# Kernel optimization log

Measured on AMD Instinct MI355X. Metric: run time of the kernel, lower is better.

## Reference

```python
import jax, jax.numpy as jnp
import numpy as np

MODEL_DIM = 2048
Q_HEADS = 32
KV_HEADS = 8
HEAD_DIM = MODEL_DIM // Q_HEADS  # 64
ROPE_BASE = 10000.0


def apply_rope(x, pos):
    # x: [B, S, H, D], interleaved-pair RoPE (torchtune-style)
    half = x.shape[-1] // 2
    inv_freq = 1.0 / (ROPE_BASE ** (jnp.arange(half, dtype=jnp.float32) * 2.0 / x.shape[-1]))
    ang = pos.astype(jnp.float32)[:, None] * inv_freq[None, :]        # [S, half]
    cos = jnp.cos(ang)[None, :, None, :]                              # [1,S,1,half]
    sin = jnp.sin(ang)[None, :, None, :]
    x1 = x[..., 0::2]
    x2 = x[..., 1::2]
    o1 = x1 * cos - x2 * sin
    o2 = x2 * cos + x1 * sin
    return jnp.stack([o1, o2], axis=-1).reshape(x.shape)


def setup_inputs() -> dict:
    key = jax.random.key(0)
    ks = jax.random.split(key, 5)
    B, S, D = 2, 2048, MODEL_DIM
    sd = 1.0 / np.sqrt(D)
    x = jax.random.normal(ks[0], (B, S, D), dtype=jnp.float32)
    wq = jax.random.normal(ks[1], (Q_HEADS * HEAD_DIM, D), dtype=jnp.float32) * sd
    wk = jax.random.normal(ks[2], (KV_HEADS * HEAD_DIM, D), dtype=jnp.float32) * sd
    wv = jax.random.normal(ks[3], (KV_HEADS * HEAD_DIM, D), dtype=jnp.float32) * sd
    wo = jax.random.normal(ks[4], (D, D), dtype=jnp.float32) * sd
    attention_mask = jnp.ones((B, S), dtype=bool)
    return {"x": x, "attention_mask": attention_mask, "wq": wq, "wk": wk, "wv": wv, "wo": wo}


def reference(x, attention_mask, wq, wk, wv, wo):
    B, S, D = x.shape
    rep = Q_HEADS // KV_HEADS
    q = (x @ wq.T).reshape(B, S, Q_HEADS, HEAD_DIM)
    k = (x @ wk.T).reshape(B, S, KV_HEADS, HEAD_DIM)
    v = (x @ wv.T).reshape(B, S, KV_HEADS, HEAD_DIM)
    # GQA repeat_interleave along head axis
    k = jnp.repeat(k, rep, axis=2)
    v = jnp.repeat(v, rep, axis=2)
    pos = jnp.arange(S)
    q = apply_rope(q, pos)
    k = apply_rope(k, pos)
    # scores [B, H, Sq, Sk]
    score = jnp.einsum('bqhd,bkhd->bhqk', q, k) / np.sqrt(HEAD_DIM)
    neg_inf = jnp.finfo(score.dtype).min
    causal = jnp.tril(jnp.ones((S, S), dtype=bool))
    score = jnp.where(causal[None, None, :, :], score, neg_inf)
    score = jnp.where(attention_mask[:, None, None, :], score, neg_inf)
    attn = jax.nn.softmax(score, axis=-1)
    out = jnp.einsum('bhqk,bkhd->bqhd', attn, v).reshape(B, S, D)
    return out @ wo.T
```

## Files before the change

### kernel.cpp

```cpp
#include <hip/hip_runtime.h>
#include <hip/hip_bf16.h>

#define S_LEN 2048
#define BATCH 2
#define DMODEL 2048
#define HQ 32
#define HKV 8
#define HD 64
#define NQ 2560
#define KDIM 2048

typedef __attribute__((ext_vector_type(8))) short bf16x8;
typedef __attribute__((ext_vector_type(4))) float f32x4;

#if __has_builtin(__builtin_amdgcn_exp2f)
#define EXP2(x) __builtin_amdgcn_exp2f(x)
#else
#define EXP2(x) exp2f(x)
#endif

template<int N> struct ic { static constexpr int value = N; };

static __device__ inline ushort f2bf(float f) {
    union { float f; unsigned u; } v; v.f = f;
    unsigned r = v.u + 0x7fff + ((v.u >> 16) & 1);
    return (ushort)(r >> 16);
}
static __device__ inline float bf2f(ushort h) {
    union { unsigned u; float f; } v; v.u = ((unsigned)h) << 16; return v.f;
}
static __device__ inline unsigned pack2(float lo, float hi) {
    return (unsigned)f2bf(lo) | ((unsigned)f2bf(hi) << 16);
}
static __device__ __forceinline__ unsigned pkbf(float lo, float hi) {
    union { float f; unsigned u; } a, b; a.f = lo; b.f = hi;
    return __builtin_amdgcn_perm(b.u + 0x8000u, a.u + 0x8000u, 0x07060302u);
}
static __device__ __forceinline__ unsigned cvtpk(float lo, float hi) {
    unsigned r;
    asm("v_cvt_pk_bf16_f32 %0, %1, %2" : "=v"(r) : "v"(lo), "v"(hi));
    return r;
}

static __device__ __forceinline__ void gload16(const ushort* g, ushort* l) {
    __builtin_amdgcn_global_load_lds(
        (const __attribute__((address_space(1))) unsigned int*)(g),
        (__attribute__((address_space(3))) unsigned int*)(l), 16, 0, 0);
}

#define BARRIER() asm volatile("s_barrier" ::: "memory")
#define WAITVM(N) asm volatile("s_waitcnt vmcnt(" #N ")" ::: "memory")

__global__ __launch_bounds__(256) void convert_kernel(const float* __restrict__ x,
                                                      const float* __restrict__ wq,
                                                      const float* __restrict__ wk,
                                                      const float* __restrict__ wv,
                                                      const float* __restrict__ wo,
                                                      ushort* __restrict__ xb,
                                                      ushort* __restrict__ wqkvb,
                                                      ushort* __restrict__ wob)
{
    size_t e = ((size_t)blockIdx.x * 256 + threadIdx.x) * 8;
    const float* src; ushort* dst;
    if (e < 8388608ul)       { src = x  + e;              dst = xb + e; }
    else if (e < 12582912ul) { src = wq + (e - 8388608);  dst = wqkvb + (e - 8388608); }
    else if (e < 13631488ul) { src = wk + (e - 12582912); dst = wqkvb + 4194304 + (e - 12582912); }
    else if (e < 14680064ul) { src = wv + (e - 13631488); dst = wqkvb + 5242880 + (e - 13631488); }
    else                     { src = wo + (e - 14680064); dst = wob + (e - 14680064); }
    float4 a = *(const float4*)src;
    float4 b = *(const float4*)(src + 4);
    uint4 p; p.x = pack2(a.x, a.y); p.y = pack2(a.z, a.w);
             p.z = pack2(b.x, b.y); p.w = pack2(b.z, b.w);
    *(uint4*)dst = p;
}

template<int BNF, int EPI>
__global__ __launch_bounds__(512, 2) void gemm256(const ushort* __restrict__ A,
                                                  const ushort* __restrict__ Bw,
                                                  ushort* __restrict__ qkv,
                                                  ushort* __restrict__ vT,
                                                  float* __restrict__ Cf)
{
    constexpr int BN = BNF * 64;
    constexpr int KT = KDIM / 64;
    __shared__ ushort As[2][256 * 64];
    __shared__ ushort Bs[2][BN * 64];
    const int t    = threadIdx.x;
    const int w    = t >> 6, lane = t & 63;
    const int quad = lane >> 4, l15 = lane & 15;
    const int l8   = lane >> 3;
    const int scw  = ((lane & 7) ^ (l8 & 7)) * 8;
    const int wm   = (w >> 2) * 128;
    const int wn   = (w & 3) * (BNF * 16);

    const int bid = blockIdx.x;
    const int sb  = (bid & 7) * 32 + (bid >> 3);
    const int mb  = (sb >> 4) * 256;
    const int nb  = (sb & 15) * BN;

    f32x4 acc[8][BNF] = {};
    bf16x8 a[4][2], b[BNF][2];

    auto SAH = [&](int buf, int half, int kb) {
        #pragma unroll
        for (int L = 0; L < 2; L++) {
            int r0 = half * 128 + (w * 2 + L) * 8;
            gload16(A + (size_t)(mb + r0 + l8) * KDIM + kb + scw, &As[buf][r0 * 64]);
        }
    };
    auto SB = [&](int buf, int kb) {
        #pragma unroll
        for (int L = 0; L < BNF; L++) {
            int r0 = (w * BNF + L) * 8;
            gload16(Bw + (size_t)(nb + r0 + l8) * KDIM + kb + scw, &Bs[buf][r0 * 64]);
        }
    };
    auto LA = [&](int buf, int hm) {
        #pragma unroll
        for (int i = 0; i < 4; i++) {
            int r = wm + hm * 64 + i * 16 + l15;
            int rs = r * 64, sw = r & 7;
            #pragma unroll
            for (int kc = 0; kc < 2; kc++)
                a[i][kc] = *(const bf16x8*)&As[buf][rs + (((kc << 2) | quad) ^ sw) * 8];
        }
    };
    auto LB = [&](int buf) {
        #pragma unroll
        for (int j = 0; j < BNF; j++) {
            int r = wn + j * 16 + l15;
            int rs = r * 64, sw = r & 7;
            #pragma unroll
            for (int kc = 0; kc < 2; kc++)
                b[j][kc] = *(const bf16x8*)&Bs[buf][rs + (((kc << 2) | quad) ^ sw) * 8];
        }
    };
    auto MM = [&](auto HM) {
        constexpr int hm = decltype(HM)::value;
        __builtin_amdgcn_s_setprio(1);
        #pragma unroll
        for (int i = 0; i < 4; i++)
            #pragma unroll
            for (int j = 0; j < BNF; j++) {
                f32x4 d = acc[hm * 4 + i][j];
                d = __builtin_amdgcn_mfma_f32_16x16x32_bf16(a[i][0], b[j][0], d, 0, 0, 0);
                d = __builtin_amdgcn_mfma_f32_16x16x32_bf16(a[i][1], b[j][1], d, 0, 0, 0);
                acc[hm * 4 + i][j] = d;
            }
        __builtin_amdgcn_s_setprio(0);
    };

    SAH(0, 0, 0); SAH(0, 1, 0); SB(0, 0);
    SAH(1, 0, 64); SB(1, 64);
    if constexpr (BNF == 3) WAITVM(5); else WAITVM(4);
    BARRIER();

    #pragma unroll 1
    for (int tt = 0; tt < KT - 2; tt++) {
        const int buf = tt & 1, o = buf ^ 1;
        LA(buf, 0); LB(buf);
        SAH(o, 1, (tt + 1) * 64);
        BARRIER();
        MM(ic<0>{});
        if constexpr (BNF == 3) WAITVM(7); else WAITVM(6);
        BARRIER();
        LA(buf, 1);
        SAH(buf, 0, (tt + 2) * 64); SB(buf, (tt + 2) * 64);
        BARRIER();
        MM(ic<1>{});
        if constexpr (BNF == 3) WAITVM(7); else WAITVM(6);
        BARRIER();
    }
    LA(0, 0); LB(0);
    SAH(1, 1, (KT - 1) * 64);
    BARRIER();
    MM(ic<0>{});
    if constexpr (BNF == 3) WAITVM(7); else WAITVM(6);
    BARRIER();
    LA(0, 1);
    BARRIER();
    MM(ic<1>{});
    WAITVM(2);
    BARRIER();
    LA(1, 0); LB(1);
    BARRIER();
    MM(ic<0>{});
    WAITVM(0);
    BARRIER();
    LA(1, 1);
    BARRIER();
    MM(ic<1>{});

    #pragma unroll
    for (int i = 0; i < 8; i++) {
        int m0 = mb + wm + (i >> 2) * 64 + (i & 3) * 16 + quad * 4;
        #pragma unroll
        for (int j = 0; j < BNF; j++) {
            int n0 = nb + wn + j * 16;
            if (EPI == 0) {
                if (n0 >= 2560) {
                    int m0p = (m0 & ~63) | (((m0 >> 5) & 1) << 5)
                            | (((m0 >> 2) & 3) << 3) | (((m0 >> 4) & 1) << 2);
                    ushort4 pk;
                    pk.x = f2bf(acc[i][j][0]); pk.y = f2bf(acc[i][j][1]);
                    pk.z = f2bf(acc[i][j][2]); pk.w = f2bf(acc[i][j][3]);
                    *(ushort4*)&vT[(size_t)(n0 + l15 - 2560) * 4096 + m0p] = pk;
                } else {
                    #pragma unroll
                    for (int r = 0; r < 4; r++)
                        qkv[(size_t)(m0 + r) * NQ + n0 + l15] = f2bf(acc[i][j][r]);
                }
            } else {
                #pragma unroll
                for (int r = 0; r < 4; r++)
                    Cf[(size_t)(m0 + r) * DMODEL + n0 + l15] = acc[i][j][r];
            }
        }
    }
}

__global__ __launch_bounds__(256) void rope_kernel(ushort* __restrict__ qkv)
{
    const int PAIRS = BATCH * S_LEN * (HQ + HKV) * (HD / 2);
    int tid = blockIdx.x * 256 + threadIdx.x;
    if (tid >= PAIRS) return;
    int token = tid / ((HQ + HKV) * 32);
    int r     = tid - token * ((HQ + HKV) * 32);
    int hh    = r >> 5;
    int i     = r & 31;
    int base  = (hh < HQ) ? hh * 64 : DMODEL + (hh - HQ) * 64;
    size_t addr = (size_t)token * NQ + base + 2 * i;
    int s = token & (S_LEN - 1);
    float freq = exp2f(-0.41524101186092f * (float)i);
    float ang  = (float)s * freq;
    float sn, cs;
    sincosf(ang, &sn, &cs);
    float x1 = bf2f(qkv[addr]);
    float x2 = bf2f(qkv[addr + 1]);
    qkv[addr]     = f2bf(x1 * cs - x2 * sn);
    qkv[addr + 1] = f2bf(x2 * cs + x1 * sn);
}

__global__ __launch_bounds__(256) void attn_kernel(const ushort* __restrict__ qkv,
                                                   const ushort* __restrict__ vT,
                                                   ushort* __restrict__ attnb)
{
    __shared__ ushort Ks[3][64 * 64];
    __shared__ ushort VT[2][64 * 64];
    const int t    = threadIdx.x;
    const int w    = t >> 6, lane = t & 63;
    const int quad = lane >> 4, l15 = lane & 15;
    const int bid  = blockIdx.x;
    const int qx   = 15 - (bid >> 6);
    const int h    = bid & 31;
    const int b    = (bid >> 5) & 1;
    const int qb   = qx * 128;
    const int kvh  = h >> 2;
    const ushort* base = qkv + (size_t)b * S_LEN * NQ;
    const ushort* vTb  = vT + (size_t)kvh * HD * 4096 + b * S_LEN;

    const float SC = 0.18033688011112042f;
    bf16x8 aq[2][2];
    #pragma unroll
    for (int h2 = 0; h2 < 2; h2++) {
        const ushort* qp = base + (size_t)(qb + w * 32 + h2 * 16 + l15) * NQ + h * HD + quad * 8;
        #pragma unroll
        for (int hf = 0; hf < 2; hf++) {
            bf16x8 v = *(const bf16x8*)(qp + hf * 32);
            #pragma unroll
            for (int j = 0; j < 8; j++) v[j] = (short)f2bf(bf2f((ushort)v[j]) * SC);
            aq[h2][hf] = v;
        }
    }

    f32x4 o[2][4] = {};
    float lsum[2] = {};
    const int qw    = qb + w * 32;
    const int strow = lane >> 3;
    const int stlc  = (lane & 7) ^ strow;
    const int niter = (qb + 128) / 64;

    auto stageK = [&](int i, int buf) {
        #pragma unroll
        for (int c = 0; c < 2; c++) {
            int key = w * 16 + c * 8 + strow;
            gload16(base + (size_t)(i * 64 + key) * NQ + DMODEL + kvh * HD + stlc * 8,
                    &Ks[buf][(w * 16 + c * 8) * 64]);
        }
    };
    auto stageV = [&](int i, int buf) {
        #pragma unroll
        for (int c = 0; c < 2; c++) {
            int key = w * 16 + c * 8 + strow;
            gload16(vTb + (size_t)key * 4096 + i * 64 + stlc * 8,
                    &VT[buf][(w * 16 + c * 8) * 64]);
        }
    };

    stageK(0, 0); stageV(0, 0); stageK(1, 1);

    int kcur = 0, vcur = 0;
    for (int i = 0; i < niter; i++) {
        const int kb = i * 64;
        if (i + 1 < niter) { WAITVM(2); } else { WAITVM(0); }
        BARRIER();
        if (i + 1 < niter) stageV(i + 1, vcur ^ 1);
        if (i + 2 < niter) stageK(i + 2, kcur >= 1 ? kcur - 1 : 2);
        if (kb <= qw + 31) {
            const bool full = (kb + 63) <= qw;
            const ushort* ks = &Ks[kcur][0];
            const ushort* vs = &VT[vcur][0];
            f32x4 s[2][4];
            #pragma unroll
            for (int kt = 0; kt < 4; kt++) {
                int key = kt * 16 + l15;
                int sw  = l15 & 7;
                bf16x8 k0 = *(const bf16x8*)&ks[key * 64 + (quad ^ sw) * 8];
                bf16x8 k1 = *(const bf16x8*)&ks[key * 64 + (((quad + 4) & 7) ^ sw) * 8];
                #pragma unroll
                for (int h2 = 0; h2 < 2; h2++) {
                    f32x4 z = {};
                    z = __builtin_amdgcn_mfma_f32_16x16x32_bf16(k0, aq[h2][0], z, 0, 0, 0);
                    z = __builtin_amdgcn_mfma_f32_16x16x32_bf16(k1, aq[h2][1], z, 0, 0, 0);
                    s[h2][kt] = z;
                }
            }
            bf16x8 pf[2][2];
            #pragma unroll
            for (int h2 = 0; h2 < 2; h2++) {
                union { unsigned u[8]; bf16x8 v[2]; } pw;
                #pragma unroll
                for (int kt = 0; kt < 4; kt++) {
                    float p0 = EXP2(s[h2][kt][0]);
                    float p1 = EXP2(s[h2][kt][1]);
                    float p2 = EXP2(s[h2][kt][2]);
                    float p3 = EXP2(s[h2][kt][3]);
                    if (!full) {
                        int key0 = kb + kt * 16 + quad * 4;
                        int q    = qb + w * 32 + h2 * 16 + l15;
                        p0 = (key0 + 0 <= q) ? p0 : 0.f;
                        p1 = (key0 + 1 <= q) ? p1 : 0.f;
                        p2 = (key0 + 2 <= q) ? p2 : 0.f;
                        p3 = (key0 + 3 <= q) ? p3 : 0.f;
                    }
                    lsum[h2] += (p0 + p1) + (p2 + p3);
                    pw.u[kt * 2 + 0] = cvtpk(p0, p1);
                    pw.u[kt * 2 + 1] = cvtpk(p2, p3);
                }
                pf[h2][0] = pw.v[0];
                pf[h2][1] = pw.v[1];
            }
            #pragma unroll
            for (int tt = 0; tt < 4; tt++) {
                int dr = tt * 16 + l15;
                int sw = l15 & 7;
                bf16x8 vf0 = *(const bf16x8*)&vs[dr * 64 + (quad ^ sw) * 8];
                bf16x8 vf1 = *(const bf16x8*)&vs[dr * 64 + (((quad + 4) & 7) ^ sw) * 8];
                #pragma unroll
                for (int h2 = 0; h2 < 2; h2++) {
                    f32x4 oo = o[h2][tt];
                    oo = __builtin_amdgcn_mfma_f32_16x16x32_bf16(vf0, pf[h2][0], oo, 0, 0, 0);
                    oo = __builtin_amdgcn_mfma_f32_16x16x32_bf16(vf1, pf[h2][1], oo, 0, 0, 0);
                    o[h2][tt] = oo;
                }
            }
        }
        kcur = (kcur + 1 == 3) ? 0 : kcur + 1;
        vcur ^= 1;
    }
    #pragma unroll
    for (int h2 = 0; h2 < 2; h2++) {
        float l = lsum[h2];
        l += __shfl_xor(l, 16, 64);
        l += __shfl_xor(l, 32, 64);
        float inv = 1.0f / l;
        ushort* ob = attnb + (size_t)(b * S_LEN + qb + w * 32 + h2 * 16 + l15) * DMODEL
                   + h * HD + quad * 4;
        #pragma unroll
        for (int tt = 0; tt < 4; tt++) {
            uint2 st;
            st.x = pkbf(o[h2][tt][0] * inv, o[h2][tt][1] * inv);
            st.y = pkbf(o[h2][tt][2] * inv, o[h2][tt][3] * inv);
            *(uint2*)&ob[tt * 16] = st;
        }
    }
}

extern "C" void kernel_launch(void* const* d_in, const int* in_sizes, int n_in,
                              void* d_out, int out_size, void* d_ws, size_t ws_size,
                              hipStream_t stream)
{
    const float* x  = (const float*)d_in[0];
    const float* wq = (const float*)d_in[2];
    const float* wk = (const float*)d_in[3];
    const float* wv = (const float*)d_in[4];
    const float* wo = (const float*)d_in[5];
    float* out = (float*)d_out;

    char* ws = (char*)d_ws;
    ushort* qkv    = (ushort*)(ws);
    ushort* vT     = (ushort*)(ws + 20971520);
    ushort* xb     = (ushort*)(ws + 25165824);
    ushort* attn_b = xb;
    ushort* wqkvb  = (ushort*)(ws + 41943040);
    ushort* wob    = (ushort*)(ws + 54525952);

    convert_kernel<<<9216, 256, 0, stream>>>(x, wq, wk, wv, wo, xb, wqkvb, wob);

    gemm256<3, 0><<<256, 512, 0, stream>>>(xb, wqkvb, qkv, vT, nullptr);

    int pairs = BATCH * S_LEN * (HQ + HKV) * (HD / 2);
    rope_kernel<<<(pairs + 255) / 256, 256, 0, stream>>>(qkv);

    attn_kernel<<<1024, 256, 0, stream>>>(qkv, vT, attn_b);

    gemm256<2, 1><<<256, 512, 0, stream>>>(attn_b, wob, nullptr, nullptr, out);
}
```

Baseline: 272.8 us.

## Stage 128-key K/V tiles with double buffering and MFMA priority hints

Restructures the attention inner loop to load 128 keys of K and V per stage into two double buffers, replacing the three-slot K ring and separate V staging at 64-key granularity. Each outer iteration runs two 64-key compute passes with one barrier and one full vmcnt wait, which halves the number of barriers and sync points. It also raises wave priority with s_setprio around the MFMA sections. The cost is more LDS per block (64KB vs 40KB), which may lower occupancy, and the wait now drains all outstanding loads rather than leaving the next tile in flight.

```diff
diff --git a/kernel.cpp b/kernel.cpp
--- a/kernel.cpp
+++ b/kernel.cpp
@@ -245,8 +245,8 @@
                                                    const ushort* __restrict__ vT,
                                                    ushort* __restrict__ attnb)
 {
-    __shared__ ushort Ks[3][64 * 64];
-    __shared__ ushort VT[2][64 * 64];
+    __shared__ ushort Ks[2][2 * 64 * 64];
+    __shared__ ushort VT[2][2 * 64 * 64];
     const int t    = threadIdx.x;
     const int w    = t >> 6, lane = t & 63;
     const int quad = lane >> 4, l15 = lane & 15;
@@ -278,95 +278,99 @@
     const int qw    = qb + w * 32;
     const int strow = lane >> 3;
     const int stlc  = (lane & 7) ^ strow;
-    const int niter = (qb + 128) / 64;
-
-    auto stageK = [&](int i, int buf) {
-        #pragma unroll
-        for (int c = 0; c < 2; c++) {
-            int key = w * 16 + c * 8 + strow;
-            gload16(base + (size_t)(i * 64 + key) * NQ + DMODEL + kvh * HD + stlc * 8,
-                    &Ks[buf][(w * 16 + c * 8) * 64]);
-        }
-    };
-    auto stageV = [&](int i, int buf) {
-        #pragma unroll
-        for (int c = 0; c < 2; c++) {
-            int key = w * 16 + c * 8 + strow;
-            gload16(vTb + (size_t)key * 4096 + i * 64 + stlc * 8,
-                    &VT[buf][(w * 16 + c * 8) * 64]);
-        }
-    };
-
-    stageK(0, 0); stageV(0, 0); stageK(1, 1);
-
-    int kcur = 0, vcur = 0;
+    const int niter = qx + 1;
+
+    auto stage = [&](int i, int buf) {
+        #pragma unroll
+        for (int c = 0; c < 4; c++) {
+            int key = w * 32 + c * 8 + strow;
+            gload16(base + (size_t)(i * 128 + key) * NQ + DMODEL + kvh * HD + stlc * 8,
+                    &Ks[buf][(w * 32 + c * 8) * 64]);
+        }
+        #pragma unroll
+        for (int s = 0; s < 2; s++)
+            #pragma unroll
+            for (int c = 0; c < 2; c++) {
+                int dr = w * 16 + c * 8 + strow;
+                gload16(vTb + (size_t)dr * 4096 + i * 128 + s * 64 + stlc * 8,
+                        &VT[buf][s * 4096 + (w * 16 + c * 8) * 64]);
+            }
+    };
+
+    auto compute = [&](const ushort* ks, const ushort* vs, int kb) {
+        const bool full = (kb + 63) <= qw;
+        f32x4 s[2][4];
+        __builtin_amdgcn_s_setprio(1);
+        #pragma unroll
+        for (int kt = 0; kt < 4; kt++) {
+            int key = kt * 16 + l15;
+            int sw  = l15 & 7;
+            bf16x8 k0 = *(const bf16x8*)&ks[key * 64 + (quad ^ sw) * 8];
+            bf16x8 k1 = *(const bf16x8*)&ks[key * 64 + (((quad + 4) & 7) ^ sw) * 8];
+            #pragma unroll
+            for (int h2 = 0; h2 < 2; h2++) {
+                f32x4 z = {};
+                z = __builtin_amdgcn_mfma_f32_16x16x32_bf16(k0, aq[h2][0], z, 0, 0, 0);
+                z = __builtin_amdgcn_mfma_f32_16x16x32_bf16(k1, aq[h2][1], z, 0, 0, 0);
+                s[h2][kt] = z;
+            }
+        }
+        __builtin_amdgcn_s_setprio(0);
+        bf16x8 pf[2][2];
+        #pragma unroll
+        for (int h2 = 0; h2 < 2; h2++) {
+            union { unsigned u[8]; bf16x8 v[2]; } pw;
+            #pragma unroll
+            for (int kt = 0; kt < 4; kt++) {
+                float p0 = EXP2(s[h2][kt][0]);
+                float p1 = EXP2(s[h2][kt][1]);
+                float p2 = EXP2(s[h2][kt][2]);
+                float p3 = EXP2(s[h2][kt][3]);
+                if (!full) {
+                    int key0 = kb + kt * 16 + quad * 4;
+                    int q    = qb + w * 32 + h2 * 16 + l15;
+                    p0 = (key0 + 0 <= q) ? p0 : 0.f;
+                    p1 = (key0 + 1 <= q) ? p1 : 0.f;
+                    p2 = (key0 + 2 <= q) ? p2 : 0.f;
+                    p3 = (key0 + 3 <= q) ? p3 : 0.f;
+                }
+                lsum[h2] += (p0 + p1) + (p2 + p3);
+                pw.u[kt * 2 + 0] = cvtpk(p0, p1);
+                pw.u[kt * 2 + 1] = cvtpk(p2, p3);
+            }
+            pf[h2][0] = pw.v[0];
+            pf[h2][1] = pw.v[1];
+        }
+        __builtin_amdgcn_s_setprio(1);
+        #pragma unroll
+        for (int tt = 0; tt < 4; tt++) {
+            int dr = tt * 16 + l15;
+            int sw = l15 & 7;
+            bf16x8 vf0 = *(const bf16x8*)&vs[dr * 64 + (quad ^ sw) * 8];
+            bf16x8 vf1 = *(const bf16x8*)&vs[dr * 64 + (((quad + 4) & 7) ^ sw) * 8];
+            #pragma unroll
+            for (int h2 = 0; h2 < 2; h2++) {
+                f32x4 oo = o[h2][tt];
+                oo = __builtin_amdgcn_mfma_f32_16x16x32_bf16(vf0, pf[h2][0], oo, 0, 0, 0);
+                oo = __builtin_amdgcn_mfma_f32_16x16x32_bf16(vf1, pf[h2][1], oo, 0, 0, 0);
+                o[h2][tt] = oo;
+            }
+        }
+        __builtin_amdgcn_s_setprio(0);
+    };
+
+    stage(0, 0);
+
     for (int i = 0; i < niter; i++) {
-        const int kb = i * 64;
-        if (i + 1 < niter) { WAITVM(2); } else { WAITVM(0); }
+        const int cur = i & 1;
+        WAITVM(0);
         BARRIER();
-        if (i + 1 < niter) stageV(i + 1, vcur ^ 1);
-        if (i + 2 < niter) stageK(i + 2, kcur >= 1 ? kcur - 1 : 2);
-        if (kb <= qw + 31) {
-            const bool full = (kb + 63) <= qw;
-            const ushort* ks = &Ks[kcur][0];
-            const ushort* vs = &VT[vcur][0];
-            f32x4 s[2][4];
-            #pragma unroll
-            for (int kt = 0; kt < 4; kt++) {
-                int key = kt * 16 + l15;
-                int sw  = l15 & 7;
-                bf16x8 k0 = *(const bf16x8*)&ks[key * 64 + (quad ^ sw) * 8];
-                bf16x8 k1 = *(const bf16x8*)&ks[key * 64 + (((quad + 4) & 7) ^ sw) * 8];
-                #pragma unroll
-                for (int h2 = 0; h2 < 2; h2++) {
-                    f32x4 z = {};
-                    z = __builtin_amdgcn_mfma_f32_16x16x32_bf16(k0, aq[h2][0], z, 0, 0, 0);
-                    z = __builtin_amdgcn_mfma_f32_16x16x32_bf16(k1, aq[h2][1], z, 0, 0, 0);
-                    s[h2][kt] = z;
-                }
-            }
-            bf16x8 pf[2][2];
-            #pragma unroll
-            for (int h2 = 0; h2 < 2; h2++) {
-                union { unsigned u[8]; bf16x8 v[2]; } pw;
-                #pragma unroll
-                for (int kt = 0; kt < 4; kt++) {
-                    float p0 = EXP2(s[h2][kt][0]);
-                    float p1 = EXP2(s[h2][kt][1]);
-                    float p2 = EXP2(s[h2][kt][2]);
-                    float p3 = EXP2(s[h2][kt][3]);
-                    if (!full) {
-                        int key0 = kb + kt * 16 + quad * 4;
-                        int q    = qb + w * 32 + h2 * 16 + l15;
-                        p0 = (key0 + 0 <= q) ? p0 : 0.f;
-                        p1 = (key0 + 1 <= q) ? p1 : 0.f;
-                        p2 = (key0 + 2 <= q) ? p2 : 0.f;
-                        p3 = (key0 + 3 <= q) ? p3 : 0.f;
-                    }
-                    lsum[h2] += (p0 + p1) + (p2 + p3);
-                    pw.u[kt * 2 + 0] = cvtpk(p0, p1);
-                    pw.u[kt * 2 + 1] = cvtpk(p2, p3);
-                }
-                pf[h2][0] = pw.v[0];
-                pf[h2][1] = pw.v[1];
-            }
-            #pragma unroll
-            for (int tt = 0; tt < 4; tt++) {
-                int dr = tt * 16 + l15;
-                int sw = l15 & 7;
-                bf16x8 vf0 = *(const bf16x8*)&vs[dr * 64 + (quad ^ sw) * 8];
-                bf16x8 vf1 = *(const bf16x8*)&vs[dr * 64 + (((quad + 4) & 7) ^ sw) * 8];
-                #pragma unroll
-                for (int h2 = 0; h2 < 2; h2++) {
-                    f32x4 oo = o[h2][tt];
-                    oo = __builtin_amdgcn_mfma_f32_16x16x32_bf16(vf0, pf[h2][0], oo, 0, 0, 0);
-                    oo = __builtin_amdgcn_mfma_f32_16x16x32_bf16(vf1, pf[h2][1], oo, 0, 0, 0);
-                    o[h2][tt] = oo;
-                }
-            }
-        }
-        kcur = (kcur + 1 == 3) ? 0 : kcur + 1;
-        vcur ^= 1;
+        if (i + 1 < niter) stage(i + 1, cur ^ 1);
+        const int kb = i * 128;
+        if (kb <= qw + 31)
+            compute(&Ks[cur][0],    &VT[cur][0],    kb);
+        if (kb + 64 <= qw + 31)
+            compute(&Ks[cur][4096], &VT[cur][4096], kb + 64);
     }
     #pragma unroll
     for (int h2 = 0; h2 < 2; h2++) {
```

Result: faster. 264.7 us (-3.0%).
